# Kernel optimization log

Hardware: AMD Instinct MI355X
Metric: run time of the kernel (lower is better)

## Reference

```python
import jax, jax.numpy as jnp
import numpy as np

NHEAD = 8

def setup_inputs() -> dict:
    key = jax.random.key(0)
    k1, k2, k3, k4 = jax.random.split(key, 4)
    B, N, I, KQ, V = 2, 4096, 512, 512, 512
    x = jax.random.normal(k1, (B, N, I), dtype=jnp.float32)
    # store weights as [in, out] so projection is x @ W (same math as torch Linear with W.T)
    Wk = jax.random.normal(k2, (I, KQ), dtype=jnp.float32) * (1.0 / np.sqrt(I))
    Wq = jax.random.normal(k3, (I, KQ), dtype=jnp.float32) * (1.0 / np.sqrt(I))
    Wv = jax.random.normal(k4, (I, V), dtype=jnp.float32) * (1.0 / np.sqrt(I))
    return {"x": x, "Wk": Wk, "Wq": Wq, "Wv": Wv}

def reference(x, Wk, Wq, Wv):
    B, N, _ = x.shape
    H = NHEAD
    k = (x @ Wk).reshape(B, N, H, -1)   # [B,N,H,dk]
    q = (x @ Wq).reshape(B, N, H, -1)   # [B,N,H,dk]
    v = (x @ Wv).reshape(B, N, H, -1)   # [B,N,H,dv]
    dk = k.shape[-1]
    # scores[b,n,m,h] = k[b,n,h,:] . q[b,m,h,:] / sqrt(dk)
    scores = jnp.einsum('bnhd,bmhd->bnmh', k, q) / jnp.sqrt(jnp.asarray(dk, x.dtype))
    attn = jax.nn.softmax(scores, axis=-2)  # softmax over m (dim -2), matching torch code
    out = jnp.einsum('bnmh,bmhd->bnhd', attn, v)
    return out.reshape(B, N, -1)
```

## Files before the change

kernel.cpp:

```cpp
#include <hip/hip_runtime.h>
#include <hip/hip_bf16.h>

typedef __bf16 bf16_t;
typedef bf16_t bf16x8 __attribute__((ext_vector_type(8)));
typedef bf16_t bf16x4 __attribute__((ext_vector_type(4)));
typedef float f32x4 __attribute__((ext_vector_type(4)));

#define MFMA16(a, b, c) __builtin_amdgcn_mfma_f32_16x16x32_bf16(a, b, c, 0, 0, 0)

typedef __attribute__((address_space(3))) unsigned int lds_u32_t;
typedef __attribute__((address_space(1))) const unsigned int glb_u32_t;

__device__ __forceinline__ void gload16(const void* g, void* l) {
    __builtin_amdgcn_global_load_lds((glb_u32_t*)g, (lds_u32_t*)l, 16, 0, 0);
}

__device__ __forceinline__ bf16x8 lds8(const bf16_t* base, int row, int cb) {
    return *reinterpret_cast<const bf16x8*>(
        reinterpret_cast<const char*>(base) + row * 128 + (cb ^ ((row & 7) << 4)));
}

__global__ __launch_bounds__(256) void convert_x(
    const float* __restrict__ X, bf16_t* __restrict__ Xb)
{
    const size_t i = ((size_t)blockIdx.x * 256 + threadIdx.x) * 8;
    const float4 v0 = *reinterpret_cast<const float4*>(&X[i]);
    const float4 v1 = *reinterpret_cast<const float4*>(&X[i + 4]);
    bf16x8 o;
    o[0] = (bf16_t)v0.x; o[1] = (bf16_t)v0.y; o[2] = (bf16_t)v0.z; o[3] = (bf16_t)v0.w;
    o[4] = (bf16_t)v1.x; o[5] = (bf16_t)v1.y; o[6] = (bf16_t)v1.z; o[7] = (bf16_t)v1.w;
    *reinterpret_cast<bf16x8*>(&Xb[i]) = o;
}

__global__ __launch_bounds__(256) void transpose_w(
    const float* __restrict__ Wq, const float* __restrict__ Wk,
    const float* __restrict__ Wv, bf16_t* __restrict__ Wt)
{
    __shared__ float T[64][65];
    const int mat = blockIdx.z;
    const float* W = (mat == 0) ? Wq : (mat == 1 ? Wk : Wv);
    const int k0 = blockIdx.x * 64, n0 = blockIdx.y * 64;
    const int r = threadIdx.x >> 4, c4 = (threadIdx.x & 15) * 4;

    for (int rep = 0; rep < 4; ++rep) {
        const int row = r + rep * 16;
        const float4 v = *reinterpret_cast<const float4*>(&W[(size_t)(k0 + row) * 512 + n0 + c4]);
        T[row][c4 + 0] = v.x; T[row][c4 + 1] = v.y;
        T[row][c4 + 2] = v.z; T[row][c4 + 3] = v.w;
    }
    __syncthreads();
    const float scl = (mat == 1) ? 0.1803368801111204f : 1.0f;
    for (int rep = 0; rep < 4; ++rep) {
        const int nrow = r + rep * 16;
        bf16x4 o;
        for (int e = 0; e < 4; ++e) o[e] = (bf16_t)(T[c4 + e][nrow] * scl);
        *reinterpret_cast<bf16x4*>(&Wt[(size_t)mat * 262144 + (size_t)(n0 + nrow) * 512 + k0 + c4]) = o;
    }
}

__global__ __launch_bounds__(256, 2) void proj_bf16(
    const bf16_t* __restrict__ Xb, const bf16_t* __restrict__ Wt,
    bf16_t* __restrict__ Qb, bf16_t* __restrict__ Kb, bf16_t* __restrict__ Vt)
{
    __shared__ bf16_t Ab[2][128 * 64];
    __shared__ bf16_t Bb[2][128 * 64];

    const int tid = threadIdx.x;
    const int w = tid >> 6, l = tid & 63, g = l >> 4, lr = l & 15;
    const int m0 = blockIdx.x * 128;
    const int mat = blockIdx.y >> 2;
    const int n0 = (blockIdx.y & 3) * 128;
    const bf16_t* Wm = Wt + (size_t)mat * 262144;
    const int wm = (w >> 1) * 64, wn = (w & 1) * 64;

#define STAGE_P(buf, k0v)                                                   \
    do {                                                                    \
        for (int t = 0; t < 4; ++t) {                                       \
            const int rb = w * 32 + t * 8;                                  \
            const int row = rb + (l >> 3);                                  \
            const int cb = ((l & 7) << 4) ^ ((row & 7) << 4);               \
            gload16(&Xb[(size_t)(m0 + row) * 512 + (k0v) + (cb >> 1)],      \
                    &Ab[buf][rb * 64]);                                     \
            gload16(&Wm[(size_t)(n0 + row) * 512 + (k0v) + (cb >> 1)],      \
                    &Bb[buf][rb * 64]);                                     \
        }                                                                   \
    } while (0)

    f32x4 acc[4][4];
    const f32x4 z4 = {0.f, 0.f, 0.f, 0.f};
#pragma unroll
    for (int i = 0; i < 4; ++i)
#pragma unroll
        for (int j = 0; j < 4; ++j) acc[i][j] = z4;

    STAGE_P(0, 0);
    __syncthreads();

    for (int kk = 0; kk < 8; ++kk) {
        const int cur = kk & 1;
        if (kk + 1 < 8) STAGE_P(cur ^ 1, (kk + 1) * 64);

        bf16x8 a[4][2], bq[4][2];
#pragma unroll
        for (int fa = 0; fa < 4; ++fa)
#pragma unroll
            for (int dh = 0; dh < 2; ++dh) {
                a[fa][dh]  = lds8(Ab[cur], wm + fa * 16 + lr, dh * 64 + g * 16);
                bq[fa][dh] = lds8(Bb[cur], wn + fa * 16 + lr, dh * 64 + g * 16);
            }
        __builtin_amdgcn_s_setprio(1);
#pragma unroll
        for (int fa = 0; fa < 4; ++fa)
#pragma unroll
            for (int fb = 0; fb < 4; ++fb) {
                acc[fa][fb] = MFMA16(a[fa][0], bq[fb][0], acc[fa][fb]);
                acc[fa][fb] = MFMA16(a[fa][1], bq[fb][1], acc[fa][fb]);
            }
        __builtin_amdgcn_s_setprio(0);
        __syncthreads();
    }
#undef STAGE_P

#pragma unroll
    for (int fa = 0; fa < 4; ++fa)
#pragma unroll
        for (int fb = 0; fb < 4; ++fb)
#pragma unroll
            for (int j = 0; j < 4; ++j) {
                const int m = m0 + wm + fa * 16 + g * 4 + j;
                const int n = n0 + wn + fb * 16 + lr;
                const bf16_t val = (bf16_t)acc[fa][fb][j];
                if (mat == 0) {
                    Qb[(size_t)m * 512 + n] = val;
                } else if (mat == 1) {
                    Kb[(size_t)m * 512 + n] = val;
                } else {
                    const int b_ = m >> 12, mm = m & 4095;
                    const int hh = n >> 6, d = n & 63;
                    const int loc = mm & 63;
                    const int mperm = (mm & ~63) | (loc & 32) |
                                      (((loc >> 2) & 3) << 3) |
                                      (((loc >> 4) & 1) << 2) | (loc & 3);
                    Vt[((size_t)((b_ * 8 + hh) * 64 + d)) * 4096 + mperm] = val;
                }
            }
}

__global__ __launch_bounds__(256) void proj_kernel(
    const float* __restrict__ X,
    const float* __restrict__ Wq, const float* __restrict__ Wk,
    const float* __restrict__ Wv,
    bf16_t* __restrict__ Qb, bf16_t* __restrict__ Kb, bf16_t* __restrict__ Vt)
{
    __shared__ bf16_t Ax[128][40];
    __shared__ bf16_t Wtl[64][40];

    const int mode = blockIdx.z;
    const float* W = (mode == 0) ? Wq : (mode == 1 ? Wk : Wv);
    bf16_t* C = (mode == 0) ? Qb : (mode == 1 ? Kb : Vt);

    const int tid = threadIdx.x;
    const int w = tid >> 6, l = tid & 63, g = l >> 4, lr = l & 15;
    const int m0 = blockIdx.x * 128, n0 = blockIdx.y * 64;

    f32x4 acc[2][4];
    const f32x4 z4 = {0.f, 0.f, 0.f, 0.f};
    for (int i = 0; i < 2; ++i)
        for (int j = 0; j < 4; ++j) acc[i][j] = z4;

    for (int k0 = 0; k0 < 512; k0 += 32) {
        {
            const int c4 = (tid & 7) * 4;
            for (int r = 0; r < 4; ++r) {
                const int row = (tid >> 3) + r * 32;
                const float4 v = *reinterpret_cast<const float4*>(
                    &X[(size_t)(m0 + row) * 512 + k0 + c4]);
                bf16x4 o;
                o[0] = (bf16_t)v.x; o[1] = (bf16_t)v.y;
                o[2] = (bf16_t)v.z; o[3] = (bf16_t)v.w;
                *reinterpret_cast<bf16x4*>(&Ax[row][c4]) = o;
            }
        }
        {
            const int c4 = (tid & 15) * 4;
            for (int r = 0; r < 2; ++r) {
                const int krow = (tid >> 4) + r * 16;
                const float4 v = *reinterpret_cast<const float4*>(
                    &W[(size_t)(k0 + krow) * 512 + n0 + c4]);
                Wtl[c4 + 0][krow] = (bf16_t)v.x;
                Wtl[c4 + 1][krow] = (bf16_t)v.y;
                Wtl[c4 + 2][krow] = (bf16_t)v.z;
                Wtl[c4 + 3][krow] = (bf16_t)v.w;
            }
        }
        __syncthreads();

        bf16x8 a[2], bq[4];
        for (int fr = 0; fr < 2; ++fr)
            a[fr] = *reinterpret_cast<const bf16x8*>(&Ax[w * 32 + fr * 16 + lr][g * 8]);
        for (int fn = 0; fn < 4; ++fn)
            bq[fn] = *reinterpret_cast<const bf16x8*>(&Wtl[fn * 16 + lr][g * 8]);
        for (int fr = 0; fr < 2; ++fr)
            for (int fn = 0; fn < 4; ++fn)
                acc[fr][fn] = MFMA16(a[fr], bq[fn], acc[fr][fn]);
        __syncthreads();
    }

    const float SCL = 0.125f * 1.44269504088896f;
    for (int fr = 0; fr < 2; ++fr)
        for (int fn = 0; fn < 4; ++fn)
            for (int j = 0; j < 4; ++j) {
                const int m = m0 + w * 32 + fr * 16 + g * 4 + j;
                const int n = n0 + fn * 16 + lr;
                float vf = acc[fr][fn][j];
                if (mode == 1) vf *= SCL;
                const bf16_t val = (bf16_t)vf;
                if (mode <= 1) {
                    C[(size_t)m * 512 + n] = val;
                } else {
                    const int b_ = m >> 12, mm = m & 4095;
                    const int hh = n >> 6, d = n & 63;
                    const int loc = mm & 63;
                    const int mperm = (mm & ~63) | (loc & 32) |
                                      (((loc >> 2) & 3) << 3) |
                                      (((loc >> 4) & 1) << 2) | (loc & 3);
                    C[((size_t)((b_ * 8 + hh) * 64 + d)) * 4096 + mperm] = val;
                }
            }
}

__global__ __launch_bounds__(512, 2) void attn_kernel(
    const bf16_t* __restrict__ Kb, const bf16_t* __restrict__ Qb,
    const bf16_t* __restrict__ Vt, float* __restrict__ Out)
{
    __shared__ __align__(16) char smem[65536];

    const int tid = threadIdx.x;
    const int w = tid >> 6, l = tid & 63, g = l >> 4, lr = l & 15;
    const int mh = w >> 2;
    const int u = w & 3;

    const int id = ((int)blockIdx.x & 7) * 64 + ((int)blockIdx.x >> 3);
    const int bh = id >> 5, nb = id & 31;
    const int b = bh >> 3, hd = bh & 7;
    const int n0 = nb * 128;
    const int t0 = mh * 32;

    bf16x8 ak[2][2];
#pragma unroll
    for (int fr = 0; fr < 2; ++fr)
#pragma unroll
        for (int dh = 0; dh < 2; ++dh)
            ak[fr][dh] = *reinterpret_cast<const bf16x8*>(
                &Kb[(size_t)(b * 4096 + n0 + u * 32 + fr * 16 + lr) * 512 +
                    hd * 64 + dh * 32 + g * 8]);

    bf16x8 ones;
#pragma unroll
    for (int i = 0; i < 8; ++i) ones[i] = (bf16_t)1.0f;

#define STAGE(buf, m0v)                                                              \
    do {                                                                             \
        char* qls = smem + mh * 32768 + (buf) * 16384;                               \
        char* vls = qls + 8192;                                                      \
        for (int t = 0; t < 2; ++t) {                                                \
            const int rb = u * 16 + t * 8;                                           \
            const int row = rb + (l >> 3);                                           \
            const int cb = ((l & 7) << 4) ^ ((row & 7) << 4);                        \
            gload16(&Qb[(size_t)(b * 4096 + (m0v) + row) * 512 + hd * 64 + (cb >> 1)],\
                    qls + rb * 128);                                                 \
            gload16(&Vt[((size_t)(bh * 64 + row)) * 4096 + (m0v) + (cb >> 1)],       \
                    vls + rb * 128);                                                 \
        }                                                                            \
    } while (0)

    f32x4 acc[2][4];
    f32x4 dacc[2];
    const f32x4 z4 = {0.f, 0.f, 0.f, 0.f};
#pragma unroll
    for (int fr = 0; fr < 2; ++fr) {
        dacc[fr] = z4;
#pragma unroll
        for (int j = 0; j < 4; ++j) acc[fr][j] = z4;
    }

    auto compute_tile = [&](int buf) {
        const bf16_t* qb = (const bf16_t*)(smem + mh * 32768 + buf * 16384);
        const bf16_t* vb = (const bf16_t*)(smem + mh * 32768 + buf * 16384 + 8192);

        f32x4 s[4][2];
#pragma unroll
        for (int m16 = 0; m16 < 4; ++m16)
#pragma unroll
            for (int fr = 0; fr < 2; ++fr) s[m16][fr] = z4;

        __builtin_amdgcn_s_setprio(1);
#pragma unroll
        for (int m16 = 0; m16 < 4; ++m16) {
            const int r = m16 * 16 + lr;
            const bf16x8 a0 = lds8(qb, r, g * 16);
            const bf16x8 a1 = lds8(qb, r, 64 + g * 16);
            s[m16][0] = MFMA16(a0, ak[0][0], s[m16][0]);
            s[m16][0] = MFMA16(a1, ak[0][1], s[m16][0]);
            s[m16][1] = MFMA16(a0, ak[1][0], s[m16][1]);
            s[m16][1] = MFMA16(a1, ak[1][1], s[m16][1]);
        }
        __builtin_amdgcn_s_setprio(0);

        bf16x8 pa[2][2];
#pragma unroll
        for (int fr = 0; fr < 2; ++fr)
#pragma unroll
            for (int c = 0; c < 2; ++c)
#pragma unroll
                for (int e = 0; e < 8; ++e)
                    pa[fr][c][e] = (bf16_t)__builtin_amdgcn_exp2f(
                        s[c * 2 + (e >> 2)][fr][e & 3]);

        __builtin_amdgcn_s_setprio(1);
        dacc[0] = MFMA16(pa[0][0], ones, dacc[0]);
        dacc[0] = MFMA16(pa[0][1], ones, dacc[0]);
        dacc[1] = MFMA16(pa[1][0], ones, dacc[1]);
        dacc[1] = MFMA16(pa[1][1], ones, dacc[1]);
#pragma unroll
        for (int fd = 0; fd < 4; ++fd) {
            const bf16x8 vb0 = lds8(vb, fd * 16 + lr, g * 16);
            const bf16x8 vb1 = lds8(vb, fd * 16 + lr, 64 + g * 16);
            acc[0][fd] = MFMA16(pa[0][0], vb0, acc[0][fd]);
            acc[0][fd] = MFMA16(pa[0][1], vb1, acc[0][fd]);
            acc[1][fd] = MFMA16(pa[1][0], vb0, acc[1][fd]);
            acc[1][fd] = MFMA16(pa[1][1], vb1, acc[1][fd]);
        }
        __builtin_amdgcn_s_setprio(0);
    };

    STAGE(0, t0 * 64);
    __syncthreads();

    for (int it = 0; it < 32; ++it) {
        if (it + 1 < 32) STAGE((it + 1) & 1, (t0 + it + 1) * 64);
        compute_tile(it & 1);
        __syncthreads();
    }

    float* comb = (float*)smem;
    float* cden = (float*)(smem + 33280);

    if (mh == 1) {
#pragma unroll
        for (int fr = 0; fr < 2; ++fr)
#pragma unroll
            for (int fd = 0; fd < 4; ++fd)
#pragma unroll
                for (int j = 0; j < 4; ++j)
                    comb[(u * 32 + fr * 16 + g * 4 + j) * 65 + fd * 16 + lr] =
                        acc[fr][fd][j];
        if (lr == 0) {
#pragma unroll
            for (int fr = 0; fr < 2; ++fr)
#pragma unroll
                for (int j = 0; j < 4; ++j)
                    cden[u * 32 + fr * 16 + g * 4 + j] = dacc[fr][j];
        }
    }
    __syncthreads();
    if (mh == 0) {
        float linv[2][4];
#pragma unroll
        for (int fr = 0; fr < 2; ++fr)
#pragma unroll
            for (int j = 0; j < 4; ++j) {
                const int nl = u * 32 + fr * 16 + g * 4 + j;
                linv[fr][j] = 1.0f / (dacc[fr][j] + cden[nl]);
            }
#pragma unroll
        for (int fr = 0; fr < 2; ++fr)
#pragma unroll
            for (int fd = 0; fd < 4; ++fd)
#pragma unroll
                for (int j = 0; j < 4; ++j) {
                    const int nl = u * 32 + fr * 16 + g * 4 + j;
                    const int d = fd * 16 + lr;
                    Out[((size_t)(b * 4096 + n0 + nl)) * 512 + hd * 64 + d] =
                        (acc[fr][fd][j] + comb[nl * 65 + d]) * linv[fr][j];
                }
    }
#undef STAGE
}

extern "C" void kernel_launch(void* const* d_in, const int* in_sizes, int n_in,
                              void* d_out, int out_size, void* d_ws, size_t ws_size,
                              hipStream_t stream)
{
    const float* x  = (const float*)d_in[0];
    const float* Wk = (const float*)d_in[1];
    const float* Wq = (const float*)d_in[2];
    const float* Wv = (const float*)d_in[3];
    float* out = (float*)d_out;

    char* ws = (char*)d_ws;
    bf16_t* Kb = (bf16_t*)ws;
    bf16_t* Qb = Kb + (size_t)4194304;
    bf16_t* Vt = Qb + (size_t)4194304;
    bf16_t* Xb = (bf16_t*)(ws + 25165824);
    bf16_t* Wt = Xb + (size_t)4194304;

    const size_t NEED_PRE = 35127296;
    const bool has_pre = ws_size >= NEED_PRE;

    if (has_pre) {
        hipLaunchKernelGGL(convert_x, dim3(2048), dim3(256), 0, stream, x, Xb);
        hipLaunchKernelGGL(transpose_w, dim3(8, 8, 3), dim3(256), 0, stream,
                           Wq, Wk, Wv, Wt);
        hipLaunchKernelGGL(proj_bf16, dim3(64, 12), dim3(256), 0, stream,
                           Xb, Wt, Qb, Kb, Vt);
    } else {
        hipLaunchKernelGGL(proj_kernel, dim3(64, 8, 3), dim3(256), 0, stream,
                           x, Wq, Wk, Wv, Qb, Kb, Vt);
    }

    hipLaunchKernelGGL(attn_kernel, dim3(512), dim3(512), 0, stream,
                       Kb, Qb, Vt, out);
}
```

Baseline: 104.2 us.

## Merge prep kernels and tile V^T layout with LDS-staged coalesced stores

Combines the x-conversion and weight-transpose kernels into a single launch to cut one kernel launch. Changes the V^T global layout to 64-column tiles stored contiguously per (bh, m-tile), and stages V output through LDS so each thread writes 16-byte coalesced chunks instead of scattered 2-byte writes. The attention kernel's V load addressing is updated to match. This adds an extra LDS round-trip and a barrier in the projection epilogue.

```diff
diff --git a/kernel.cpp b/kernel.cpp
--- a/kernel.cpp
+++ b/kernel.cpp
@@ -20,26 +20,28 @@
         reinterpret_cast<const char*>(base) + row * 128 + (cb ^ ((row & 7) << 4)));
 }
 
-__global__ __launch_bounds__(256) void convert_x(
-    const float* __restrict__ X, bf16_t* __restrict__ Xb)
-{
-    const size_t i = ((size_t)blockIdx.x * 256 + threadIdx.x) * 8;
-    const float4 v0 = *reinterpret_cast<const float4*>(&X[i]);
-    const float4 v1 = *reinterpret_cast<const float4*>(&X[i + 4]);
-    bf16x8 o;
-    o[0] = (bf16_t)v0.x; o[1] = (bf16_t)v0.y; o[2] = (bf16_t)v0.z; o[3] = (bf16_t)v0.w;
-    o[4] = (bf16_t)v1.x; o[5] = (bf16_t)v1.y; o[6] = (bf16_t)v1.z; o[7] = (bf16_t)v1.w;
-    *reinterpret_cast<bf16x8*>(&Xb[i]) = o;
-}
-
-__global__ __launch_bounds__(256) void transpose_w(
+__global__ __launch_bounds__(256) void prep_kernel(
+    const float* __restrict__ X,
     const float* __restrict__ Wq, const float* __restrict__ Wk,
-    const float* __restrict__ Wv, bf16_t* __restrict__ Wt)
+    const float* __restrict__ Wv,
+    bf16_t* __restrict__ Xb, bf16_t* __restrict__ Wt)
 {
     __shared__ float T[64][65];
-    const int mat = blockIdx.z;
+    if (blockIdx.x < 2048) {
+        const size_t i = ((size_t)blockIdx.x * 256 + threadIdx.x) * 8;
+        const float4 v0 = *reinterpret_cast<const float4*>(&X[i]);
+        const float4 v1 = *reinterpret_cast<const float4*>(&X[i + 4]);
+        bf16x8 o;
+        o[0] = (bf16_t)v0.x; o[1] = (bf16_t)v0.y; o[2] = (bf16_t)v0.z; o[3] = (bf16_t)v0.w;
+        o[4] = (bf16_t)v1.x; o[5] = (bf16_t)v1.y; o[6] = (bf16_t)v1.z; o[7] = (bf16_t)v1.w;
+        *reinterpret_cast<bf16x8*>(&Xb[i]) = o;
+        return;
+    }
+    const int idx = (int)blockIdx.x - 2048;
+    const int mat = idx >> 6;
+    const int rem = idx & 63;
+    const int k0 = (rem >> 3) * 64, n0 = (rem & 7) * 64;
     const float* W = (mat == 0) ? Wq : (mat == 1 ? Wk : Wv);
-    const int k0 = blockIdx.x * 64, n0 = blockIdx.y * 64;
     const int r = threadIdx.x >> 4, c4 = (threadIdx.x & 15) * 4;
 
     for (int rep = 0; rep < 4; ++rep) {
@@ -62,8 +64,9 @@
     const bf16_t* __restrict__ Xb, const bf16_t* __restrict__ Wt,
     bf16_t* __restrict__ Qb, bf16_t* __restrict__ Kb, bf16_t* __restrict__ Vt)
 {
-    __shared__ bf16_t Ab[2][128 * 64];
-    __shared__ bf16_t Bb[2][128 * 64];
+    __shared__ __align__(16) char smemP[65536];
+    bf16_t* Ab0 = (bf16_t*)smemP;
+    bf16_t* Bb0 = (bf16_t*)(smemP + 32768);
 
     const int tid = threadIdx.x;
     const int w = tid >> 6, l = tid & 63, g = l >> 4, lr = l & 15;
@@ -80,9 +83,9 @@
             const int row = rb + (l >> 3);                                  \
             const int cb = ((l & 7) << 4) ^ ((row & 7) << 4);               \
             gload16(&Xb[(size_t)(m0 + row) * 512 + (k0v) + (cb >> 1)],      \
-                    &Ab[buf][rb * 64]);                                     \
+                    Ab0 + (buf) * 8192 + rb * 64);                          \
             gload16(&Wm[(size_t)(n0 + row) * 512 + (k0v) + (cb >> 1)],      \
-                    &Bb[buf][rb * 64]);                                     \
+                    Bb0 + (buf) * 8192 + rb * 64);                          \
         }                                                                   \
     } while (0)
 
@@ -105,8 +108,8 @@
         for (int fa = 0; fa < 4; ++fa)
 #pragma unroll
             for (int dh = 0; dh < 2; ++dh) {
-                a[fa][dh]  = lds8(Ab[cur], wm + fa * 16 + lr, dh * 64 + g * 16);
-                bq[fa][dh] = lds8(Bb[cur], wn + fa * 16 + lr, dh * 64 + g * 16);
+                a[fa][dh]  = lds8(Ab0 + cur * 8192, wm + fa * 16 + lr, dh * 64 + g * 16);
+                bq[fa][dh] = lds8(Bb0 + cur * 8192, wn + fa * 16 + lr, dh * 64 + g * 16);
             }
         __builtin_amdgcn_s_setprio(1);
 #pragma unroll
@@ -121,29 +124,59 @@
     }
 #undef STAGE_P
 
+    if (mat <= 1) {
+        bf16_t* C = (mat == 0) ? Qb : Kb;
+#pragma unroll
+        for (int fa = 0; fa < 4; ++fa)
+#pragma unroll
+            for (int fb = 0; fb < 4; ++fb) {
+                bf16x4 v4;
+#pragma unroll
+                for (int j = 0; j < 4; ++j) v4[j] = (bf16_t)acc[fa][fb][j];
+#pragma unroll
+                for (int j = 0; j < 4; ++j) {
+                    const int m = m0 + wm + fa * 16 + g * 4 + j;
+                    const int n = n0 + wn + fb * 16 + lr;
+                    C[(size_t)m * 512 + n] = v4[j];
+                }
+            }
+        return;
+    }
+
+    bf16_t* vt_lds = (bf16_t*)smemP;
 #pragma unroll
     for (int fa = 0; fa < 4; ++fa)
 #pragma unroll
-        for (int fb = 0; fb < 4; ++fb)
-#pragma unroll
-            for (int j = 0; j < 4; ++j) {
-                const int m = m0 + wm + fa * 16 + g * 4 + j;
-                const int n = n0 + wn + fb * 16 + lr;
-                const bf16_t val = (bf16_t)acc[fa][fb][j];
-                if (mat == 0) {
-                    Qb[(size_t)m * 512 + n] = val;
-                } else if (mat == 1) {
-                    Kb[(size_t)m * 512 + n] = val;
-                } else {
-                    const int b_ = m >> 12, mm = m & 4095;
-                    const int hh = n >> 6, d = n & 63;
-                    const int loc = mm & 63;
-                    const int mperm = (mm & ~63) | (loc & 32) |
-                                      (((loc >> 2) & 3) << 3) |
-                                      (((loc >> 4) & 1) << 2) | (loc & 3);
-                    Vt[((size_t)((b_ * 8 + hh) * 64 + d)) * 4096 + mperm] = val;
-                }
-            }
+        for (int fb = 0; fb < 4; ++fb) {
+            const int ml = wm + fa * 16 + g * 4;
+            const int loc = ml & 63;
+            const int p = (loc & 32) | (((loc >> 2) & 3) << 3) |
+                          (((loc >> 4) & 1) << 2) | (loc & 3);
+            const int col = ((ml >> 6) << 6) + p;
+            const int nl = wn + fb * 16 + lr;
+            bf16x4 v4;
+#pragma unroll
+            for (int j = 0; j < 4; ++j) v4[j] = (bf16_t)acc[fa][fb][j];
+            *reinterpret_cast<bf16x4*>(&vt_lds[nl * 132 + col]) = v4;
+        }
+    __syncthreads();
+
+    const int hh0 = n0 >> 6;
+    const int b_ = m0 >> 12;
+    const int mt0 = (m0 & 4095) >> 6;
+#pragma unroll
+    for (int pass = 0; pass < 8; ++pass) {
+        const int unit = pass * 32 + w * 8 + (l >> 3);
+        const int row = unit & 127;
+        const int mt_half = unit >> 7;
+        const int d = row & 63, hh = hh0 + (row >> 6);
+        const int bh_ = b_ * 8 + hh;
+        const int mt = mt0 + mt_half;
+        const bf16x8 v8 = *reinterpret_cast<const bf16x8*>(
+            &vt_lds[row * 132 + mt_half * 64 + (l & 7) * 8]);
+        *reinterpret_cast<bf16x8*>(
+            &Vt[(size_t)bh_ * 262144 + (size_t)mt * 4096 + d * 64 + (l & 7) * 8]) = v8;
+    }
 }
 
 __global__ __launch_bounds__(256) void proj_kernel(
@@ -221,10 +254,10 @@
                     const int b_ = m >> 12, mm = m & 4095;
                     const int hh = n >> 6, d = n & 63;
                     const int loc = mm & 63;
-                    const int mperm = (mm & ~63) | (loc & 32) |
-                                      (((loc >> 2) & 3) << 3) |
-                                      (((loc >> 4) & 1) << 2) | (loc & 3);
-                    C[((size_t)((b_ * 8 + hh) * 64 + d)) * 4096 + mperm] = val;
+                    const int p = (loc & 32) | (((loc >> 2) & 3) << 3) |
+                                  (((loc >> 4) & 1) << 2) | (loc & 3);
+                    C[(size_t)(b_ * 8 + hh) * 262144 +
+                      (size_t)(mm >> 6) * 4096 + d * 64 + p] = val;
                 }
             }
 }
@@ -264,13 +297,13 @@
         char* qls = smem + mh * 32768 + (buf) * 16384;                               \
         char* vls = qls + 8192;                                                      \
         for (int t = 0; t < 2; ++t) {                                                \
-            const int rb = u * 16 + t * 8;                                           \
-            const int row = rb + (l >> 3);                                           \
+            const int row = u * 16 + t * 8 + (l >> 3);                               \
             const int cb = ((l & 7) << 4) ^ ((row & 7) << 4);                        \
             gload16(&Qb[(size_t)(b * 4096 + (m0v) + row) * 512 + hd * 64 + (cb >> 1)],\
-                    qls + rb * 128);                                                 \
-            gload16(&Vt[((size_t)(bh * 64 + row)) * 4096 + (m0v) + (cb >> 1)],       \
-                    vls + rb * 128);                                                 \
+                    qls + (u * 16 + t * 8) * 128);                                   \
+            gload16(&Vt[(size_t)bh * 262144 + (size_t)((m0v) >> 6) * 4096 +          \
+                        row * 64 + (cb >> 1)],                                       \
+                    vls + (u * 16 + t * 8) * 128);                                   \
         }                                                                            \
     } while (0)
 
@@ -409,9 +442,8 @@
     const bool has_pre = ws_size >= NEED_PRE;
 
     if (has_pre) {
-        hipLaunchKernelGGL(convert_x, dim3(2048), dim3(256), 0, stream, x, Xb);
-        hipLaunchKernelGGL(transpose_w, dim3(8, 8, 3), dim3(256), 0, stream,
-                           Wq, Wk, Wv, Wt);
+        hipLaunchKernelGGL(prep_kernel, dim3(2240), dim3(256), 0, stream,
+                           x, Wq, Wk, Wv, Xb, Wt);
         hipLaunchKernelGGL(proj_bf16, dim3(64, 12), dim3(256), 0, stream,
                            Xb, Wt, Qb, Kb, Vt);
     } else {
```

Measured after the change: 90.39 us. -13.2%, faster.
